# Kernel tuning notes

Hardware: AMD Instinct MI355X
Metric: run time of the kernel (lower is better)

Reference implementation:

```python
import jax, jax.numpy as jnp
import numpy as np

DEPTH = 6
HEADS = 12
DIM_HEAD = 64
ROT_DIM = 32  # rotary applied to first 32 dims of each head


def _ln(x, g, b, eps=1e-5):
    m = x.mean(-1, keepdims=True)
    v = ((x - m) ** 2).mean(-1, keepdims=True)
    return (x - m) * jax.lax.rsqrt(v + eps) * g + b


def _rope(x, inv_freq):
    # x: [b, h, n, DIM_HEAD]; rotate first ROT_DIM dims, interleaved-pair convention
    n = x.shape[2]
    t = jnp.arange(n, dtype=x.dtype)
    freqs = t[:, None] * inv_freq[None, :]          # [n, ROT_DIM//2]
    freqs = jnp.repeat(freqs, 2, axis=-1)           # [n, ROT_DIM]
    cos, sin = jnp.cos(freqs), jnp.sin(freqs)
    x1, x2 = x[..., :ROT_DIM], x[..., ROT_DIM:]
    xr = x1.reshape(*x1.shape[:-1], ROT_DIM // 2, 2)
    half = jnp.stack([-xr[..., 1], xr[..., 0]], axis=-1).reshape(x1.shape)
    return jnp.concatenate([x1 * cos + half * sin, x2], axis=-1)


def setup_inputs() -> dict:
    key = jax.random.key(0)
    ks = jax.random.split(key, 16)
    b, n, pd, d, mlp = 2, 1023, 768, 768, 3072
    inner = HEADS * DIM_HEAD
    s = 0.02
    inp = {}
    inp['filaments'] = jax.random.normal(ks[0], (b, n, pd), jnp.float32)
    inp['mask'] = jnp.ones((b, HEADS, n + 1, n + 1), jnp.float32)
    # patch embedding: LN -> Linear -> LN
    inp['ln_p1_g'] = jnp.ones((pd,), jnp.float32)
    inp['ln_p1_b'] = jnp.zeros((pd,), jnp.float32)
    inp['W_patch'] = jax.random.normal(ks[1], (pd, d), jnp.float32) * s
    inp['b_patch'] = jnp.zeros((d,), jnp.float32)
    inp['ln_p2_g'] = jnp.ones((d,), jnp.float32)
    inp['ln_p2_b'] = jnp.zeros((d,), jnp.float32)
    # PEG depthwise conv1d, k=3
    inp['peg_w'] = jax.random.normal(ks[2], (d, 1, 3), jnp.float32) * s
    inp['peg_b'] = jnp.zeros((d,), jnp.float32)
    inp['cls_token'] = jax.random.normal(ks[3], (1, 1, d), jnp.float32)
    # shared attention (weight-tied across depth)
    inp['ln_a_g'] = jnp.ones((DEPTH, d), jnp.float32)
    inp['ln_a_b'] = jnp.zeros((DEPTH, d), jnp.float32)
    inp['W_qkv'] = jax.random.normal(ks[4], (d, 3 * inner), jnp.float32) * s
    inp['W_o'] = jax.random.normal(ks[5], (inner, d), jnp.float32) * s
    inp['b_o'] = jnp.zeros((d,), jnp.float32)
    inp['inv_freq'] = (1.0 / (10000.0 ** (jnp.arange(0, ROT_DIM, 2, dtype=jnp.float32) / ROT_DIM)))
    # per-layer FFN
    inp['ln_f_g'] = jnp.ones((DEPTH, d), jnp.float32)
    inp['ln_f_b'] = jnp.zeros((DEPTH, d), jnp.float32)
    inp['W1'] = jax.random.normal(ks[6], (DEPTH, d, mlp), jnp.float32) * s
    inp['b1'] = jnp.zeros((DEPTH, mlp), jnp.float32)
    inp['W2'] = jax.random.normal(ks[7], (DEPTH, mlp, d), jnp.float32) * s
    inp['b2'] = jnp.zeros((DEPTH, d), jnp.float32)
    return inp


def reference(filaments, mask, ln_p1_g, ln_p1_b, W_patch, b_patch, ln_p2_g, ln_p2_b,
              peg_w, peg_b, cls_token, ln_a_g, ln_a_b, W_qkv, W_o, b_o, inv_freq,
              ln_f_g, ln_f_b, W1, b1, W2, b2):
    b = filaments.shape[0]
    d = W_patch.shape[1]
    x = _ln(filaments, ln_p1_g, ln_p1_b) @ W_patch + b_patch
    x = _ln(x, ln_p2_g, ln_p2_b)
    x = jnp.concatenate([jnp.broadcast_to(cls_token, (b, 1, d)), x], axis=1)  # [b, n+1, d]
    # PEG: depthwise conv over sequence, residual add
    xc = jnp.transpose(x, (0, 2, 1))  # NCW
    peg = jax.lax.conv_general_dilated(xc, peg_w, (1,), 'SAME',
                                       dimension_numbers=('NCH', 'OIH', 'NCH'),
                                       feature_group_count=d)
    x = x + jnp.transpose(peg, (0, 2, 1)) + peg_b
    add_mask = (1.0 - mask) * (-1e9)
    scale = DIM_HEAD ** -0.5
    n1 = x.shape[1]
    for i in range(DEPTH):
        h = _ln(x, ln_a_g[i], ln_a_b[i])
        qkv = h @ W_qkv
        q, k, v = jnp.split(qkv, 3, axis=-1)
        def to_heads(t):
            return t.reshape(b, n1, HEADS, DIM_HEAD).transpose(0, 2, 1, 3)
        q, k, v = to_heads(q), to_heads(k), to_heads(v)
        q = _rope(q, inv_freq)
        k = _rope(k, inv_freq)
        dots = jnp.einsum('bhid,bhjd->bhij', q, k) * scale + add_mask
        attn = jax.nn.softmax(dots, axis=-1)
        o = jnp.einsum('bhij,bhjd->bhid', attn, v).transpose(0, 2, 1, 3).reshape(b, n1, -1)
        x = o @ W_o + b_o + x
        h = _ln(x, ln_f_g[i], ln_f_b[i])
        x = jax.nn.gelu(h @ W1[i] + b1[i], approximate=False) @ W2[i] + b2[i] + x
    return x
```

## Files before the change

kernel.cpp:

```cpp
#include <hip/hip_runtime.h>
#include <hip/hip_bf16.h>
#include <math.h>

typedef __attribute__((ext_vector_type(8))) short          bf16x8;
typedef __attribute__((ext_vector_type(8))) unsigned short ushort8;
typedef __attribute__((ext_vector_type(4))) float          f32x4;

__device__ __forceinline__ unsigned short f2bf(float f) {
    union { float f; unsigned u; } v; v.f = f;
    unsigned u = v.u;
    unsigned r = (u + 0x7FFFu + ((u >> 16) & 1u)) >> 16;
    return (unsigned short)r;
}
__device__ __forceinline__ float bf2f(unsigned short h) {
    union { unsigned u; float f; } v; v.u = ((unsigned)h) << 16;
    return v.f;
}

__device__ __forceinline__ void gload16(const void* g, void* l) {
    __builtin_amdgcn_global_load_lds(
        (const __attribute__((address_space(1))) void*)g,
        (__attribute__((address_space(3))) void*)l, 16, 0, 0);
}

__global__ __launch_bounds__(256) void wt_cast_k(const float* __restrict__ in,
                                                 unsigned short* __restrict__ out,
                                                 int K, int N) {
    __shared__ float t[64][65];
    in  += (size_t)blockIdx.z * K * N;
    out += (size_t)blockIdx.z * K * N;
    int n0 = blockIdx.x * 64, k0 = blockIdx.y * 64;
    int tx = threadIdx.x & 63, ty = threadIdx.x >> 6;
    #pragma unroll
    for (int p = 0; p < 16; ++p) {
        int k = ty + p * 4;
        t[k][tx] = in[(size_t)(k0 + k) * N + n0 + tx];
    }
    __syncthreads();
    #pragma unroll
    for (int p = 0; p < 16; ++p) {
        int n = ty + p * 4;
        out[(size_t)(n0 + n) * K + k0 + tx] = f2bf(t[tx][n]);
    }
}

__global__ __launch_bounds__(256) void cossin_k(const float* __restrict__ inv_freq,
                                                float* __restrict__ cosT,
                                                float* __restrict__ sinT) {
    int idx = blockIdx.x * 256 + threadIdx.x;
    int t = idx >> 4, p = idx & 15;
    float fr = (float)t * inv_freq[p];
    cosT[idx] = cosf(fr);
    sinT[idx] = sinf(fr);
}

__global__ __launch_bounds__(256) void mask_flags_k(const float* __restrict__ mask,
                                                    unsigned char* __restrict__ flags) {
    int idx = blockIdx.x;
    int tid = threadIdx.x;
    int kt = idx & 15, qt = (idx >> 4) & 15, bh = idx >> 8;
    int r = tid >> 2, cc = (tid & 3) * 16;
    const float* prow = mask + ((size_t)bh * 1024 + (size_t)qt * 64 + r) * 1024 + kt * 64 + cc;
    int bad = 0;
    #pragma unroll
    for (int j = 0; j < 4; ++j) {
        float4 v = *(const float4*)(prow + j * 4);
        bad |= (v.x != 1.f) || (v.y != 1.f) || (v.z != 1.f) || (v.w != 1.f);
    }
    __shared__ int sb[4];
    unsigned long long anyb = __ballot(bad != 0);
    if ((tid & 63) == 0) sb[tid >> 6] = (anyb != 0ull) ? 1 : 0;
    __syncthreads();
    if (tid == 0) flags[idx] = (unsigned char)(!(sb[0] | sb[1] | sb[2] | sb[3]));
}

__global__ __launch_bounds__(256) void ln768_bf_k(const float* __restrict__ in,
                                                  const float* __restrict__ g,
                                                  const float* __restrict__ b,
                                                  unsigned short* __restrict__ out,
                                                  int Mvalid) {
    int r = blockIdx.x, tid = threadIdx.x;
    unsigned short* y = out + (size_t)r * 768;
    if (r >= Mvalid) { y[tid] = 0; y[tid + 256] = 0; y[tid + 512] = 0; return; }
    const float* x = in + (size_t)r * 768;
    float v0 = x[tid], v1 = x[tid + 256], v2 = x[tid + 512];
    __shared__ float red[4];
    float s = v0 + v1 + v2;
    #pragma unroll
    for (int off = 32; off > 0; off >>= 1) s += __shfl_down(s, off);
    if ((tid & 63) == 0) red[tid >> 6] = s;
    __syncthreads();
    float mean = (red[0] + red[1] + red[2] + red[3]) * (1.0f / 768.0f);
    float d0 = v0 - mean, d1 = v1 - mean, d2 = v2 - mean;
    float q = d0 * d0 + d1 * d1 + d2 * d2;
    __syncthreads();
    #pragma unroll
    for (int off = 32; off > 0; off >>= 1) q += __shfl_down(q, off);
    if ((tid & 63) == 0) red[tid >> 6] = q;
    __syncthreads();
    float var = (red[0] + red[1] + red[2] + red[3]) * (1.0f / 768.0f);
    float rs = rsqrtf(var + 1e-5f);
    y[tid]       = f2bf(d0 * rs * g[tid]       + b[tid]);
    y[tid + 256] = f2bf(d1 * rs * g[tid + 256] + b[tid + 256]);
    y[tid + 512] = f2bf(d2 * rs * g[tid + 512] + b[tid + 512]);
}

__global__ __launch_bounds__(256) void ln768_k(const float* __restrict__ in,
                                               const float* __restrict__ g,
                                               const float* __restrict__ b,
                                               float* __restrict__ out,
                                               int remap) {
    int r = blockIdx.x, tid = threadIdx.x;
    const float* x = in + (size_t)r * 768;
    float v0 = x[tid], v1 = x[tid + 256], v2 = x[tid + 512];
    __shared__ float red[4];
    float s = v0 + v1 + v2;
    #pragma unroll
    for (int off = 32; off > 0; off >>= 1) s += __shfl_down(s, off);
    if ((tid & 63) == 0) red[tid >> 6] = s;
    __syncthreads();
    float mean = (red[0] + red[1] + red[2] + red[3]) * (1.0f / 768.0f);
    float d0 = v0 - mean, d1 = v1 - mean, d2 = v2 - mean;
    float q = d0 * d0 + d1 * d1 + d2 * d2;
    __syncthreads();
    #pragma unroll
    for (int off = 32; off > 0; off >>= 1) q += __shfl_down(q, off);
    if ((tid & 63) == 0) red[tid >> 6] = q;
    __syncthreads();
    float var = (red[0] + red[1] + red[2] + red[3]) * (1.0f / 768.0f);
    float rs = rsqrtf(var + 1e-5f);
    int orow = remap ? ((r / 1023) * 1024 + 1 + (r % 1023)) : r;
    float* y = out + (size_t)orow * 768;
    y[tid]       = d0 * rs * g[tid]       + b[tid];
    y[tid + 256] = d1 * rs * g[tid + 256] + b[tid + 256];
    y[tid + 512] = d2 * rs * g[tid + 512] + b[tid + 512];
}

__global__ void cls_k(const float* __restrict__ cls, float* __restrict__ x) {
    int bi = blockIdx.x, tid = threadIdx.x;
    #pragma unroll
    for (int k = 0; k < 3; ++k)
        x[(size_t)bi * 1024 * 768 + tid + k * 256] = cls[tid + k * 256];
}

__global__ __launch_bounds__(256) void peg_ln_k(const float* __restrict__ x,
                                                const float* __restrict__ w,
                                                const float* __restrict__ pb,
                                                float* __restrict__ y,
                                                const float* __restrict__ g,
                                                const float* __restrict__ b,
                                                unsigned short* __restrict__ obf) {
    int r = blockIdx.x;
    int i = r & 1023;
    int tid = threadIdx.x;
    const float* xr = x + (size_t)r * 768;
    float* yr = y + (size_t)r * 768;
    float v[3];
    #pragma unroll
    for (int k = 0; k < 3; ++k) {
        int d = tid + k * 256;
        float c  = xr[d];
        float lf = (i > 0)    ? xr[d - 768] : 0.f;
        float rt = (i < 1023) ? xr[d + 768] : 0.f;
        v[k] = c + pb[d] + w[d * 3 + 0] * lf + w[d * 3 + 1] * c + w[d * 3 + 2] * rt;
        yr[d] = v[k];
    }
    __shared__ float red[4];
    float s = v[0] + v[1] + v[2];
    #pragma unroll
    for (int off = 32; off > 0; off >>= 1) s += __shfl_down(s, off);
    if ((tid & 63) == 0) red[tid >> 6] = s;
    __syncthreads();
    float mean = (red[0] + red[1] + red[2] + red[3]) * (1.0f / 768.0f);
    float d0 = v[0] - mean, d1 = v[1] - mean, d2 = v[2] - mean;
    float q = d0 * d0 + d1 * d1 + d2 * d2;
    __syncthreads();
    #pragma unroll
    for (int off = 32; off > 0; off >>= 1) q += __shfl_down(q, off);
    if ((tid & 63) == 0) red[tid >> 6] = q;
    __syncthreads();
    float var = (red[0] + red[1] + red[2] + red[3]) * (1.0f / 768.0f);
    float rs = rsqrtf(var + 1e-5f);
    unsigned short* yb = obf + (size_t)r * 768;
    yb[tid]       = f2bf(d0 * rs * g[tid]       + b[tid]);
    yb[tid + 256] = f2bf(d1 * rs * g[tid + 256] + b[tid + 256]);
    yb[tid + 512] = f2bf(d2 * rs * g[tid + 512] + b[tid + 512]);
}

__global__ __launch_bounds__(256) void attn_mfma_k(const unsigned short* __restrict__ qkv,
                                                   const float* __restrict__ mask,
                                                   const unsigned char* __restrict__ flags,
                                                   unsigned short* __restrict__ o) {
    const int qt = blockIdx.x, bh = blockIdx.y;
    const int bi = bh / 12, h = bh % 12;
    const int tid = threadIdx.x;
    const int w = tid >> 6, lane = tid & 63;
    const int l16 = lane & 15, lq = lane >> 4;

    __shared__ unsigned short lK[64 * 64];
    __shared__ unsigned short lV[64 * 64];

    const int q0 = qt * 64;
    const size_t tokbase = (size_t)bi * 1024;
    const int qrow = q0 + w * 16 + l16;

    bf16x8 qb[2];
    {
        const unsigned short* qp = qkv + (tokbase + qrow) * 2304 + h * 64;
        qb[0] = *(const bf16x8*)(qp + lq * 8);
        qb[1] = *(const bf16x8*)(qp + 32 + lq * 8);
    }

    const float* mrow = mask + ((size_t)bh * 1024 + qrow) * 1024;
    const unsigned char* fl = flags + ((size_t)bh * 16 + qt) * 16;

    float m_run = -1e30f, l_run = 0.f;
    f32x4 oacc[4] = {};

    for (int kt = 0; kt < 16; ++kt) {
        const int k0 = kt * 64;
        const bool triv = fl[kt] != 0;
        {
            const unsigned short* krp = qkv + (tokbase + k0 + lane) * 2304 + 768 + h * 64 + w * 16;
            const unsigned short* vrp = krp + 768;
            ushort8 kA = *(const ushort8*)krp, kB = *(const ushort8*)(krp + 8);
            ushort8 vA = *(const ushort8*)vrp, vB = *(const ushort8*)(vrp + 8);
            int byA = lane * 128 + ((w * 32 +  0) ^ ((lane & 7) << 4));
            int byB = lane * 128 + ((w * 32 + 16) ^ ((lane & 7) << 4));
            *(ushort8*)((char*)lK + byA) = kA;
            *(ushort8*)((char*)lK + byB) = kB;
            #pragma unroll
            for (int j = 0; j < 16; ++j) {
                int row = w * 16 + j;
                int by = row * 128 + ((2 * lane) ^ ((row & 7) << 4));
                *(unsigned short*)((char*)lV + by) = (j < 8) ? (unsigned short)vA[j] : (unsigned short)vB[j - 8];
            }
        }
        __syncthreads();

        f32x4 sacc[4] = {};
        #pragma unroll
        for (int f = 0; f < 4; ++f) {
            int krow = f * 16 + l16;
            #pragma unroll
            for (int s = 0; s < 2; ++s) {
                int by = krow * 128 + (((s * 64) + lq * 16) ^ ((krow & 7) << 4));
                bf16x8 af = *(const bf16x8*)((const char*)lK + by);
                sacc[f] = __builtin_amdgcn_mfma_f32_16x16x32_bf16(af, qb[s], sacc[f], 0, 0, 0);
            }
        }

        float pv[4][4];
        float smax = -1e30f;
        if (triv) {
            #pragma unroll
            for (int f = 0; f < 4; ++f) {
                pv[f][0] = sacc[f][0] * 0.125f;
                pv[f][1] = sacc[f][1] * 0.125f;
                pv[f][2] = sacc[f][2] * 0.125f;
                pv[f][3] = sacc[f][3] * 0.125f;
                smax = fmaxf(smax, fmaxf(fmaxf(pv[f][0], pv[f][1]), fmaxf(pv[f][2], pv[f][3])));
            }
        } else {
            #pragma unroll
            for (int f = 0; f < 4; ++f) {
                float4 mk = *(const float4*)(mrow + k0 + f * 16 + lq * 4);
                pv[f][0] = sacc[f][0] * 0.125f + (1.f - mk.x) * -1e9f;
                pv[f][1] = sacc[f][1] * 0.125f + (1.f - mk.y) * -1e9f;
                pv[f][2] = sacc[f][2] * 0.125f + (1.f - mk.z) * -1e9f;
                pv[f][3] = sacc[f][3] * 0.125f + (1.f - mk.w) * -1e9f;
                smax = fmaxf(smax, fmaxf(fmaxf(pv[f][0], pv[f][1]), fmaxf(pv[f][2], pv[f][3])));
            }
        }
        smax = fmaxf(smax, __shfl_xor(smax, 16));
        smax = fmaxf(smax, __shfl_xor(smax, 32));
        float m_new = fmaxf(m_run, smax);
        float fac = expf(m_run - m_new);
        float lsum = 0.f;
        #pragma unroll
        for (int f = 0; f < 4; ++f) {
            #pragma unroll
            for (int i = 0; i < 4; ++i) {
                pv[f][i] = expf(pv[f][i] - m_new);
                lsum += pv[f][i];
            }
        }
        lsum += __shfl_xor(lsum, 16);
        lsum += __shfl_xor(lsum, 32);
        l_run = l_run * fac + lsum;
        m_run = m_new;

        #pragma unroll
        for (int i = 0; i < 4; ++i) {
            float fi = __shfl(fac, 4 * lq + i);
            oacc[0][i] *= fi; oacc[1][i] *= fi; oacc[2][i] *= fi; oacc[3][i] *= fi;
        }

        unsigned wpk[4][2];
        #pragma unroll
        for (int f = 0; f < 4; ++f) {
            wpk[f][0] = (unsigned)f2bf(pv[f][0]) | ((unsigned)f2bf(pv[f][1]) << 16);
            wpk[f][1] = (unsigned)f2bf(pv[f][2]) | ((unsigned)f2bf(pv[f][3]) << 16);
        }

        #pragma unroll
        for (int s = 0; s < 2; ++s) {
            unsigned aw[4];
            #pragma unroll
            for (int t = 0; t < 4; ++t) {
                int src = (2 * (lq & 1) + (t >> 1)) * 16 + l16;
                unsigned lo = __shfl(wpk[2 * s][t & 1], src);
                unsigned hi = __shfl(wpk[2 * s + 1][t & 1], src);
                aw[t] = (lq >> 1) ? hi : lo;
            }
            union { unsigned u[4]; bf16x8 v; } pa;
            pa.u[0] = aw[0]; pa.u[1] = aw[1]; pa.u[2] = aw[2]; pa.u[3] = aw[3];
            #pragma unroll
            for (int f = 0; f < 4; ++f) {
                int drow = f * 16 + l16;
                int by = drow * 128 + (((s * 64) + lq * 16) ^ ((drow & 7) << 4));
                bf16x8 vb = *(const bf16x8*)((const char*)lV + by);
                oacc[f] = __builtin_amdgcn_mfma_f32_16x16x32_bf16(pa.v, vb, oacc[f], 0, 0, 0);
            }
        }
        __syncthreads();
    }

    #pragma unroll
    for (int i = 0; i < 4; ++i) {
        float li = __shfl(l_run, 4 * lq + i);
        float inv = 1.f / li;
        int row = q0 + w * 16 + 4 * lq + i;
        unsigned short* op = o + (tokbase + row) * 768 + h * 64 + l16;
        #pragma unroll
        for (int f = 0; f < 4; ++f)
            op[f * 16] = f2bf(oacc[f][i] * inv);
    }
}

template<bool GELU, bool OBF16, bool ROPE>
__global__ __launch_bounds__(256) void gemm64_k(const unsigned short* __restrict__ A,
                                                const unsigned short* __restrict__ Bt,
                                                const float* __restrict__ bias,
                                                const float* __restrict__ res,
                                                void* __restrict__ Cv,
                                                const float* __restrict__ cosT,
                                                const float* __restrict__ sinT,
                                                int M, int N, int K) {
    __shared__ unsigned short lA[2][64 * 64];
    __shared__ unsigned short lB[2][64 * 64];
    int tid = threadIdx.x;
    int m0 = blockIdx.y * 64, n0 = blockIdx.x * 64;
    int w = tid >> 6, lane = tid & 63;
    int l16 = lane & 15, lq = lane >> 4;
    int wrow = (w >> 1) * 32, wcol = (w & 1) * 32;

    f32x4 acc[2][2] = {};

    auto stage = [&](int buf, int k0) {
        #pragma unroll
        for (int i = 0; i < 2; ++i) {
            int ch = tid + i * 256;
            int r = ch >> 3, c = ch & 7;
            int cs = c ^ (r & 7);
            gload16(A + (size_t)(m0 + r) * K + k0 + cs * 8, &lA[buf][ch * 8]);
        }
        #pragma unroll
        for (int i = 0; i < 2; ++i) {
            int ch = tid + i * 256;
            int r = ch >> 3, c = ch & 7;
            int cs = c ^ (r & 7);
            gload16(Bt + (size_t)(n0 + r) * K + k0 + cs * 8, &lB[buf][ch * 8]);
        }
    };

    const int nk = K >> 6;
    stage(0, 0);
    __syncthreads();
    int cur = 0;
    for (int t = 0; t < nk; ++t) {
        if (t + 1 < nk) stage(cur ^ 1, (t + 1) << 6);
        #pragma unroll
        for (int ks = 0; ks < 2; ++ks) {
            bf16x8 af[2], bfv[2];
            #pragma unroll
            for (int fm = 0; fm < 2; ++fm) {
                int row = wrow + fm * 16 + l16;
                int by = row * 128 + ((ks * 64 + lq * 16) ^ ((row & 7) << 4));
                af[fm] = *(const bf16x8*)((const char*)&lA[cur][0] + by);
            }
            #pragma unroll
            for (int fn = 0; fn < 2; ++fn) {
                int row = wcol + fn * 16 + l16;
                int by = row * 128 + ((ks * 64 + lq * 16) ^ ((row & 7) << 4));
                bfv[fn] = *(const bf16x8*)((const char*)&lB[cur][0] + by);
            }
            #pragma unroll
            for (int fm = 0; fm < 2; ++fm)
                #pragma unroll
                for (int fn = 0; fn < 2; ++fn)
                    acc[fm][fn] = __builtin_amdgcn_mfma_f32_16x16x32_bf16(af[fm], bfv[fn], acc[fm][fn], 0, 0, 0);
        }
        __syncthreads();
        cur ^= 1;
    }

    float* Cf = (float*)Cv;
    unsigned short* Cb = (unsigned short*)Cv;
    #pragma unroll
    for (int fm = 0; fm < 2; ++fm)
        #pragma unroll
        for (int fn = 0; fn < 2; ++fn) {
            int col = n0 + wcol + fn * 16 + l16;
            float bv = bias ? bias[col] : 0.f;
            bool rot = ROPE && (col < 1536) && ((wcol + fn * 16) < 32);
            int pidx = (wcol + fn * 16 + l16) >> 1;
            #pragma unroll
            for (int i = 0; i < 4; ++i) {
                int row = m0 + wrow + fm * 16 + 4 * lq + i;
                float v = acc[fm][fn][i];
                if (ROPE) {
                    float pr = __shfl_xor(v, 1);
                    if (rot) {
                        int tt = (row & 1023) * 16 + pidx;
                        float c = cosT[tt], s = sinT[tt];
                        v = (l16 & 1) ? (v * c + pr * s) : (v * c - pr * s);
                    }
                }
                if (row < M) {
                    v += bv;
                    if (GELU) v = 0.5f * v * (1.0f + erff(v * 0.70710678118f));
                    if (res)  v += res[(size_t)row * N + col];
                    if (OBF16) Cb[(size_t)row * N + col] = f2bf(v);
                    else       Cf[(size_t)row * N + col] = v;
                }
            }
        }
}

__global__ __launch_bounds__(256) void gemm64_splitk_k(const unsigned short* __restrict__ A,
                                                       const unsigned short* __restrict__ Bt,
                                                       float* __restrict__ P,
                                                       int M, int N, int Ktot, int Kc) {
    __shared__ unsigned short lA[2][64 * 64];
    __shared__ unsigned short lB[2][64 * 64];
    int tid = threadIdx.x;
    int m0 = blockIdx.y * 64, n0 = blockIdx.x * 64;
    int kb = blockIdx.z * Kc;
    int w = tid >> 6, lane = tid & 63;
    int l16 = lane & 15, lq = lane >> 4;
    int wrow = (w >> 1) * 32, wcol = (w & 1) * 32;

    f32x4 acc[2][2] = {};

    auto stage = [&](int buf, int k0) {
        #pragma unroll
        for (int i = 0; i < 2; ++i) {
            int ch = tid + i * 256;
            int r = ch >> 3, c = ch & 7;
            int cs = c ^ (r & 7);
            gload16(A + (size_t)(m0 + r) * Ktot + k0 + cs * 8, &lA[buf][ch * 8]);
        }
        #pragma unroll
        for (int i = 0; i < 2; ++i) {
            int ch = tid + i * 256;
            int r = ch >> 3, c = ch & 7;
            int cs = c ^ (r & 7);
            gload16(Bt + (size_t)(n0 + r) * Ktot + k0 + cs * 8, &lB[buf][ch * 8]);
        }
    };

    const int nk = Kc >> 6;
    stage(0, kb);
    __syncthreads();
    int cur = 0;
    for (int t = 0; t < nk; ++t) {
        if (t + 1 < nk) stage(cur ^ 1, kb + ((t + 1) << 6));
        #pragma unroll
        for (int ks = 0; ks < 2; ++ks) {
            bf16x8 af[2], bfv[2];
            #pragma unroll
            for (int fm = 0; fm < 2; ++fm) {
                int row = wrow + fm * 16 + l16;
                int by = row * 128 + ((ks * 64 + lq * 16) ^ ((row & 7) << 4));
                af[fm] = *(const bf16x8*)((const char*)&lA[cur][0] + by);
            }
            #pragma unroll
            for (int fn = 0; fn < 2; ++fn) {
                int row = wcol + fn * 16 + l16;
                int by = row * 128 + ((ks * 64 + lq * 16) ^ ((row & 7) << 4));
                bfv[fn] = *(const bf16x8*)((const char*)&lB[cur][0] + by);
            }
            #pragma unroll
            for (int fm = 0; fm < 2; ++fm)
                #pragma unroll
                for (int fn = 0; fn < 2; ++fn)
                    acc[fm][fn] = __builtin_amdgcn_mfma_f32_16x16x32_bf16(af[fm], bfv[fn], acc[fm][fn], 0, 0, 0);
        }
        __syncthreads();
        cur ^= 1;
    }

    float* Pz = P + (size_t)blockIdx.z * M * N;
    #pragma unroll
    for (int fm = 0; fm < 2; ++fm)
        #pragma unroll
        for (int fn = 0; fn < 2; ++fn) {
            int col = n0 + wcol + fn * 16 + l16;
            #pragma unroll
            for (int i = 0; i < 4; ++i) {
                int row = m0 + wrow + fm * 16 + 4 * lq + i;
                Pz[(size_t)row * N + col] = acc[fm][fn][i];
            }
        }
}

template<int NP>
__global__ __launch_bounds__(256) void redsum_ln_k(const float* __restrict__ P,
                                                   const float* __restrict__ bias,
                                                   const float* __restrict__ res,
                                                   float* __restrict__ outf,
                                                   const float* __restrict__ g,
                                                   const float* __restrict__ b,
                                                   unsigned short* __restrict__ obf) {
    const int MN = 2048 * 768;
    int r = blockIdx.x, tid = threadIdx.x;
    float v[3];
    #pragma unroll
    for (int j = 0; j < 3; ++j) {
        int col = tid + j * 256;
        size_t idx = (size_t)r * 768 + col;
        float a = res[idx] + bias[col];
        #pragma unroll
        for (int pz = 0; pz < NP; ++pz)
            a += P[(size_t)pz * MN + idx];
        v[j] = a;
        outf[idx] = a;
    }
    if (!g) return;
    __shared__ float red[4];
    float s = v[0] + v[1] + v[2];
    #pragma unroll
    for (int off = 32; off > 0; off >>= 1) s += __shfl_down(s, off);
    if ((tid & 63) == 0) red[tid >> 6] = s;
    __syncthreads();
    float mean = (red[0] + red[1] + red[2] + red[3]) * (1.0f / 768.0f);
    float d0 = v[0] - mean, d1 = v[1] - mean, d2 = v[2] - mean;
    float q = d0 * d0 + d1 * d1 + d2 * d2;
    __syncthreads();
    #pragma unroll
    for (int off = 32; off > 0; off >>= 1) q += __shfl_down(q, off);
    if ((tid & 63) == 0) red[tid >> 6] = q;
    __syncthreads();
    float var = (red[0] + red[1] + red[2] + red[3]) * (1.0f / 768.0f);
    float rs = rsqrtf(var + 1e-5f);
    unsigned short* yb = obf + (size_t)r * 768;
    yb[tid]       = f2bf(d0 * rs * g[tid]       + b[tid]);
    yb[tid + 256] = f2bf(d1 * rs * g[tid + 256] + b[tid + 256]);
    yb[tid + 512] = f2bf(d2 * rs * g[tid + 512] + b[tid + 512]);
}

extern "C" void kernel_launch(void* const* d_in, const int* in_sizes, int n_in,
                              void* d_out, int out_size, void* d_ws, size_t ws_size,
                              hipStream_t stream) {
    const float* filaments = (const float*)d_in[0];
    const float* mask      = (const float*)d_in[1];
    const float* ln_p1_g   = (const float*)d_in[2];
    const float* ln_p1_b   = (const float*)d_in[3];
    const float* W_patch   = (const float*)d_in[4];
    const float* b_patch   = (const float*)d_in[5];
    const float* ln_p2_g   = (const float*)d_in[6];
    const float* ln_p2_b   = (const float*)d_in[7];
    const float* peg_w     = (const float*)d_in[8];
    const float* peg_b     = (const float*)d_in[9];
    const float* cls_token = (const float*)d_in[10];
    const float* ln_a_g    = (const float*)d_in[11];
    const float* ln_a_b    = (const float*)d_in[12];
    const float* W_qkv     = (const float*)d_in[13];
    const float* W_o       = (const float*)d_in[14];
    const float* b_o       = (const float*)d_in[15];
    const float* inv_freq  = (const float*)d_in[16];
    const float* ln_f_g    = (const float*)d_in[17];
    const float* ln_f_b    = (const float*)d_in[18];
    const float* W1        = (const float*)d_in[19];
    const float* b1        = (const float*)d_in[20];
    const float* W2        = (const float*)d_in[21];
    const float* b2        = (const float*)d_in[22];

    char* p = (char*)d_ws;
    float* xa            = (float*)p;          p += 2048 * 768 * 4;
    float* xb            = (float*)p;          p += 2048 * 768 * 4;
    unsigned short* h_bf = (unsigned short*)p; p += 2048 * 768 * 2;
    unsigned short* qkv  = (unsigned short*)p; p += 2048 * 3072 * 2;
    float* Pbuf          = (float*)p;          p += (size_t)4 * 2048 * 768 * 4;
    unsigned short* w1t  = (unsigned short*)p; p += (size_t)6 * 3072 * 768 * 2;
    unsigned short* w2t  = (unsigned short*)p; p += (size_t)6 * 3072 * 768 * 2;
    unsigned short* wqt  = (unsigned short*)p; p += 2304 * 768 * 2;
    unsigned short* wot  = (unsigned short*)p; p += 768 * 768 * 2;
    unsigned short* wpt  = (unsigned short*)p; p += 768 * 768 * 2;
    float* cosT          = (float*)p;          p += 16384 * 4;
    float* sinT          = (float*)p;          p += 16384 * 4;
    unsigned char* flags = (unsigned char*)p;  p += 8192;
    unsigned short* m_bf = qkv;
    float* tmp = (float*)qkv;
    float* out = (float*)d_out;

    mask_flags_k<<<6144, 256, 0, stream>>>(mask, flags);
    cossin_k<<<64, 256, 0, stream>>>(inv_freq, cosT, sinT);
    wt_cast_k<<<dim3(12, 12), 256, 0, stream>>>(W_patch, wpt, 768, 768);
    wt_cast_k<<<dim3(36, 12), 256, 0, stream>>>(W_qkv,  wqt, 768, 2304);
    wt_cast_k<<<dim3(12, 12), 256, 0, stream>>>(W_o,    wot, 768, 768);
    wt_cast_k<<<dim3(48, 12, 6), 256, 0, stream>>>(W1, w1t, 768, 3072);
    wt_cast_k<<<dim3(12, 48, 6), 256, 0, stream>>>(W2, w2t, 3072, 768);

    ln768_bf_k<<<2048, 256, 0, stream>>>(filaments, ln_p1_g, ln_p1_b, h_bf, 2046);
    gemm64_k<false, false, false><<<dim3(12, 32), 256, 0, stream>>>(h_bf, wpt, b_patch, nullptr, tmp,
                                                                    nullptr, nullptr, 2046, 768, 768);
    ln768_k<<<2046, 256, 0, stream>>>(tmp, ln_p2_g, ln_p2_b, xa, 1);
    cls_k<<<2, 256, 0, stream>>>(cls_token, xa);
    peg_ln_k<<<2048, 256, 0, stream>>>(xa, peg_w, peg_b, xb, ln_a_g, ln_a_b, h_bf);

    float* cur = xb;
    float* nxt = xa;
    for (int i = 0; i < 6; ++i) {
        gemm64_k<false, true, true><<<dim3(36, 32), 256, 0, stream>>>(h_bf, wqt, nullptr, nullptr, qkv,
                                                                      cosT, sinT, 2048, 2304, 768);
        attn_mfma_k<<<dim3(16, 24), 256, 0, stream>>>(qkv, mask, flags, h_bf);
        gemm64_splitk_k<<<dim3(12, 32, 2), 256, 0, stream>>>(h_bf, wot, Pbuf, 2048, 768, 768, 384);
        redsum_ln_k<2><<<2048, 256, 0, stream>>>(Pbuf, b_o, cur, nxt,
                                                 ln_f_g + i * 768, ln_f_b + i * 768, h_bf);
        gemm64_k<true, true, false><<<dim3(48, 32), 256, 0, stream>>>(h_bf, w1t + (size_t)i * 3072 * 768, b1 + i * 3072,
                                                                      nullptr, m_bf, nullptr, nullptr, 2048, 3072, 768);
        gemm64_splitk_k<<<dim3(12, 32, 4), 256, 0, stream>>>(m_bf, w2t + (size_t)i * 768 * 3072, Pbuf, 2048, 768, 3072, 768);
        redsum_ln_k<4><<<2048, 256, 0, stream>>>(Pbuf, b2 + i * 768, nxt, (i == 5) ? out : cur,
                                                 (i < 5) ? (ln_a_g + (i + 1) * 768) : nullptr,
                                                 (i < 5) ? (ln_a_b + (i + 1) * 768) : nullptr, h_bf);
    }
}
```

Baseline: 941.6 us.

## Use three-stage LDS pipeline with explicit vmcnt waits in GEMM kernels

Replaces the double-buffered GEMM main loop with a triple-buffered pipeline that keeps two tiles in flight. It waits with explicit s_waitcnt vmcnt counts plus a single barrier per iteration, where before it synchronised after each compute step. The aim is to hide global-to-LDS load latency behind MFMA work. It raises LDS use to 48KB per block, which may lower occupancy, and it relies on the compiler's vmcnt accounting matching the hand-written counts.

```diff
diff --git a/kernel.cpp b/kernel.cpp
--- a/kernel.cpp
+++ b/kernel.cpp
@@ -338,6 +338,69 @@
     }
 }
 
+#define GEMM64_PIPE(A_, Bt_, KSTRIDE_, KBASE_, NK_)                                   \
+    auto stage = [&](int buf, int t) {                                                \
+        int k0 = (KBASE_) + (t << 6);                                                 \
+        {                                                                             \
+            int ch = tid, r = ch >> 3, c = ch & 7;                                    \
+            int cs = c ^ (r & 7);                                                     \
+            gload16((A_) + (size_t)(m0 + r) * (KSTRIDE_) + k0 + cs * 8,               \
+                    &lA[buf][ch * 8]);                                                \
+        }                                                                             \
+        {                                                                             \
+            int ch = tid + 256, r = ch >> 3, c = ch & 7;                              \
+            int cs = c ^ (r & 7);                                                     \
+            gload16((A_) + (size_t)(m0 + r) * (KSTRIDE_) + k0 + cs * 8,               \
+                    &lA[buf][ch * 8]);                                                \
+        }                                                                             \
+        {                                                                             \
+            int ch = tid, r = ch >> 3, c = ch & 7;                                    \
+            int cs = c ^ (r & 7);                                                     \
+            gload16((Bt_) + (size_t)(n0 + r) * (KSTRIDE_) + k0 + cs * 8,              \
+                    &lB[buf][ch * 8]);                                                \
+        }                                                                             \
+        {                                                                             \
+            int ch = tid + 256, r = ch >> 3, c = ch & 7;                              \
+            int cs = c ^ (r & 7);                                                     \
+            gload16((Bt_) + (size_t)(n0 + r) * (KSTRIDE_) + k0 + cs * 8,              \
+                    &lB[buf][ch * 8]);                                                \
+        }                                                                             \
+    };                                                                                \
+    const int nk = (NK_);                                                             \
+    stage(0, 0);                                                                      \
+    stage(1, 1);                                                                      \
+    int rd = 0, wr = 2;                                                               \
+    for (int t = 0; t < nk; ++t) {                                                    \
+        if (t + 1 < nk) asm volatile("s_waitcnt vmcnt(4)" ::: "memory");              \
+        else            asm volatile("s_waitcnt vmcnt(0)" ::: "memory");              \
+        __builtin_amdgcn_s_barrier();                                                 \
+        if (t + 2 < nk) stage(wr, t + 2);                                             \
+        _Pragma("unroll")                                                             \
+        for (int ks = 0; ks < 2; ++ks) {                                              \
+            bf16x8 af[2], bfv[2];                                                     \
+            _Pragma("unroll")                                                         \
+            for (int fm = 0; fm < 2; ++fm) {                                          \
+                int row = wrow + fm * 16 + l16;                                       \
+                int by = row * 128 + ((ks * 64 + lq * 16) ^ ((row & 7) << 4));        \
+                af[fm] = *(const bf16x8*)((const char*)&lA[rd][0] + by);              \
+            }                                                                         \
+            _Pragma("unroll")                                                         \
+            for (int fn = 0; fn < 2; ++fn) {                                          \
+                int row = wcol + fn * 16 + l16;                                       \
+                int by = row * 128 + ((ks * 64 + lq * 16) ^ ((row & 7) << 4));        \
+                bfv[fn] = *(const bf16x8*)((const char*)&lB[rd][0] + by);             \
+            }                                                                         \
+            _Pragma("unroll")                                                         \
+            for (int fm = 0; fm < 2; ++fm)                                            \
+                _Pragma("unroll")                                                     \
+                for (int fn = 0; fn < 2; ++fn)                                        \
+                    acc[fm][fn] = __builtin_amdgcn_mfma_f32_16x16x32_bf16(            \
+                        af[fm], bfv[fn], acc[fm][fn], 0, 0, 0);                       \
+        }                                                                             \
+        rd = (rd == 2) ? 0 : rd + 1;                                                  \
+        wr = (wr == 2) ? 0 : wr + 1;                                                  \
+    }
+
 template<bool GELU, bool OBF16, bool ROPE>
 __global__ __launch_bounds__(256) void gemm64_k(const unsigned short* __restrict__ A,
                                                 const unsigned short* __restrict__ Bt,
@@ -347,8 +410,8 @@
                                                 const float* __restrict__ cosT,
                                                 const float* __restrict__ sinT,
                                                 int M, int N, int K) {
-    __shared__ unsigned short lA[2][64 * 64];
-    __shared__ unsigned short lB[2][64 * 64];
+    __shared__ unsigned short lA[3][64 * 64];
+    __shared__ unsigned short lB[3][64 * 64];
     int tid = threadIdx.x;
     int m0 = blockIdx.y * 64, n0 = blockIdx.x * 64;
     int w = tid >> 6, lane = tid & 63;
@@ -357,53 +420,7 @@
 
     f32x4 acc[2][2] = {};
 
-    auto stage = [&](int buf, int k0) {
-        #pragma unroll
-        for (int i = 0; i < 2; ++i) {
-            int ch = tid + i * 256;
-            int r = ch >> 3, c = ch & 7;
-            int cs = c ^ (r & 7);
-            gload16(A + (size_t)(m0 + r) * K + k0 + cs * 8, &lA[buf][ch * 8]);
-        }
-        #pragma unroll
-        for (int i = 0; i < 2; ++i) {
-            int ch = tid + i * 256;
-            int r = ch >> 3, c = ch & 7;
-            int cs = c ^ (r & 7);
-            gload16(Bt + (size_t)(n0 + r) * K + k0 + cs * 8, &lB[buf][ch * 8]);
-        }
-    };
-
-    const int nk = K >> 6;
-    stage(0, 0);
-    __syncthreads();
-    int cur = 0;
-    for (int t = 0; t < nk; ++t) {
-        if (t + 1 < nk) stage(cur ^ 1, (t + 1) << 6);
-        #pragma unroll
-        for (int ks = 0; ks < 2; ++ks) {
-            bf16x8 af[2], bfv[2];
-            #pragma unroll
-            for (int fm = 0; fm < 2; ++fm) {
-                int row = wrow + fm * 16 + l16;
-                int by = row * 128 + ((ks * 64 + lq * 16) ^ ((row & 7) << 4));
-                af[fm] = *(const bf16x8*)((const char*)&lA[cur][0] + by);
-            }
-            #pragma unroll
-            for (int fn = 0; fn < 2; ++fn) {
-                int row = wcol + fn * 16 + l16;
-                int by = row * 128 + ((ks * 64 + lq * 16) ^ ((row & 7) << 4));
-                bfv[fn] = *(const bf16x8*)((const char*)&lB[cur][0] + by);
-            }
-            #pragma unroll
-            for (int fm = 0; fm < 2; ++fm)
-                #pragma unroll
-                for (int fn = 0; fn < 2; ++fn)
-                    acc[fm][fn] = __builtin_amdgcn_mfma_f32_16x16x32_bf16(af[fm], bfv[fn], acc[fm][fn], 0, 0, 0);
-        }
-        __syncthreads();
-        cur ^= 1;
-    }
+    GEMM64_PIPE(A, Bt, K, 0, K >> 6)
 
     float* Cf = (float*)Cv;
     unsigned short* Cb = (unsigned short*)Cv;
@@ -442,8 +459,8 @@
                                                        const unsigned short* __restrict__ Bt,
                                                        float* __restrict__ P,
                                                        int M, int N, int Ktot, int Kc) {
-    __shared__ unsigned short lA[2][64 * 64];
-    __shared__ unsigned short lB[2][64 * 64];
+    __shared__ unsigned short lA[3][64 * 64];
+    __shared__ unsigned short lB[3][64 * 64];
     int tid = threadIdx.x;
     int m0 = blockIdx.y * 64, n0 = blockIdx.x * 64;
     int kb = blockIdx.z * Kc;
@@ -453,53 +470,7 @@
 
     f32x4 acc[2][2] = {};
 
-    auto stage = [&](int buf, int k0) {
-        #pragma unroll
-        for (int i = 0; i < 2; ++i) {
-            int ch = tid + i * 256;
-            int r = ch >> 3, c = ch & 7;
-            int cs = c ^ (r & 7);
-            gload16(A + (size_t)(m0 + r) * Ktot + k0 + cs * 8, &lA[buf][ch * 8]);
-        }
-        #pragma unroll
-        for (int i = 0; i < 2; ++i) {
-            int ch = tid + i * 256;
-            int r = ch >> 3, c = ch & 7;
-            int cs = c ^ (r & 7);
-            gload16(Bt + (size_t)(n0 + r) * Ktot + k0 + cs * 8, &lB[buf][ch * 8]);
-        }
-    };
-
-    const int nk = Kc >> 6;
-    stage(0, kb);
-    __syncthreads();
-    int cur = 0;
-    for (int t = 0; t < nk; ++t) {
-        if (t + 1 < nk) stage(cur ^ 1, kb + ((t + 1) << 6));
-        #pragma unroll
-        for (int ks = 0; ks < 2; ++ks) {
-            bf16x8 af[2], bfv[2];
-            #pragma unroll
-            for (int fm = 0; fm < 2; ++fm) {
-                int row = wrow + fm * 16 + l16;
-                int by = row * 128 + ((ks * 64 + lq * 16) ^ ((row & 7) << 4));
-                af[fm] = *(const bf16x8*)((const char*)&lA[cur][0] + by);
-            }
-            #pragma unroll
-            for (int fn = 0; fn < 2; ++fn) {
-                int row = wcol + fn * 16 + l16;
-                int by = row * 128 + ((ks * 64 + lq * 16) ^ ((row & 7) << 4));
-                bfv[fn] = *(const bf16x8*)((const char*)&lB[cur][0] + by);
-            }
-            #pragma unroll
-            for (int fm = 0; fm < 2; ++fm)
-                #pragma unroll
-                for (int fn = 0; fn < 2; ++fn)
-                    acc[fm][fn] = __builtin_amdgcn_mfma_f32_16x16x32_bf16(af[fm], bfv[fn], acc[fm][fn], 0, 0, 0);
-        }
-        __syncthreads();
-        cur ^= 1;
-    }
+    GEMM64_PIPE(A, Bt, Ktot, kb, Kc >> 6)
 
     float* Pz = P + (size_t)blockIdx.z * M * N;
     #pragma unroll
```

After: 966.2 us. 2.6% more time.

## Double-buffer K/V tiles in attention kernel to overlap global loads with MFMA

Applied to the files above, without the earlier changes.

The attention kernel now keeps two LDS buffers each for K and V. The next tile's global loads are issued into registers before the QK^T and PV MFMAs on the current tile, and are written to the alternate buffer afterwards. This hides global load latency behind compute and removes one __syncthreads per iteration. In exchange it doubles LDS use to 32KB per block, which may lower occupancy, and keeps the prefetched values live in registers across the compute.

```diff
diff --git a/kernel.cpp b/kernel.cpp
--- a/kernel.cpp
+++ b/kernel.cpp
@@ -197,8 +197,8 @@
     const int w = tid >> 6, lane = tid & 63;
     const int l16 = lane & 15, lq = lane >> 4;
 
-    __shared__ unsigned short lK[64 * 64];
-    __shared__ unsigned short lV[64 * 64];
+    __shared__ unsigned short lK[2][64 * 64];
+    __shared__ unsigned short lV[2][64 * 64];
 
     const int q0 = qt * 64;
     const size_t tokbase = (size_t)bi * 1024;
@@ -214,29 +214,38 @@
     const float* mrow = mask + ((size_t)bh * 1024 + qrow) * 1024;
     const unsigned char* fl = flags + ((size_t)bh * 16 + qt) * 16;
 
+    const int byA = lane * 128 + ((w * 32 +  0) ^ ((lane & 7) << 4));
+    const int byB = lane * 128 + ((w * 32 + 16) ^ ((lane & 7) << 4));
+
     float m_run = -1e30f, l_run = 0.f;
     f32x4 oacc[4] = {};
 
+    {
+        const unsigned short* krp = qkv + (tokbase + lane) * 2304 + 768 + h * 64 + w * 16;
+        ushort8 kA = *(const ushort8*)krp, kB = *(const ushort8*)(krp + 8);
+        ushort8 vA = *(const ushort8*)(krp + 768), vB = *(const ushort8*)(krp + 776);
+        *(ushort8*)((char*)&lK[0][0] + byA) = kA;
+        *(ushort8*)((char*)&lK[0][0] + byB) = kB;
+        #pragma unroll
+        for (int j = 0; j < 16; ++j) {
+            int row = w * 16 + j;
+            int by = row * 128 + ((2 * lane) ^ ((row & 7) << 4));
+            *(unsigned short*)((char*)&lV[0][0] + by) = (j < 8) ? (unsigned short)vA[j] : (unsigned short)vB[j - 8];
+        }
+    }
+
     for (int kt = 0; kt < 16; ++kt) {
-        const int k0 = kt * 64;
+        const int cur = kt & 1;
         const bool triv = fl[kt] != 0;
-        {
-            const unsigned short* krp = qkv + (tokbase + k0 + lane) * 2304 + 768 + h * 64 + w * 16;
-            const unsigned short* vrp = krp + 768;
-            ushort8 kA = *(const ushort8*)krp, kB = *(const ushort8*)(krp + 8);
-            ushort8 vA = *(const ushort8*)vrp, vB = *(const ushort8*)(vrp + 8);
-            int byA = lane * 128 + ((w * 32 +  0) ^ ((lane & 7) << 4));
-            int byB = lane * 128 + ((w * 32 + 16) ^ ((lane & 7) << 4));
-            *(ushort8*)((char*)lK + byA) = kA;
-            *(ushort8*)((char*)lK + byB) = kB;
-            #pragma unroll
-            for (int j = 0; j < 16; ++j) {
-                int row = w * 16 + j;
-                int by = row * 128 + ((2 * lane) ^ ((row & 7) << 4));
-                *(unsigned short*)((char*)lV + by) = (j < 8) ? (unsigned short)vA[j] : (unsigned short)vB[j - 8];
-            }
-        }
         __syncthreads();
+
+        ushort8 kA, kB, vA, vB;
+        const bool have_next = (kt + 1) < 16;
+        if (have_next) {
+            const unsigned short* krp = qkv + (tokbase + (kt + 1) * 64 + lane) * 2304 + 768 + h * 64 + w * 16;
+            kA = *(const ushort8*)krp;       kB = *(const ushort8*)(krp + 8);
+            vA = *(const ushort8*)(krp + 768); vB = *(const ushort8*)(krp + 776);
+        }
 
         f32x4 sacc[4] = {};
         #pragma unroll
@@ -245,7 +254,7 @@
             #pragma unroll
             for (int s = 0; s < 2; ++s) {
                 int by = krow * 128 + (((s * 64) + lq * 16) ^ ((krow & 7) << 4));
-                bf16x8 af = *(const bf16x8*)((const char*)lK + by);
+                bf16x8 af = *(const bf16x8*)((const char*)&lK[cur][0] + by);
                 sacc[f] = __builtin_amdgcn_mfma_f32_16x16x32_bf16(af, qb[s], sacc[f], 0, 0, 0);
             }
         }
@@ -264,7 +273,7 @@
         } else {
             #pragma unroll
             for (int f = 0; f < 4; ++f) {
-                float4 mk = *(const float4*)(mrow + k0 + f * 16 + lq * 4);
+                float4 mk = *(const float4*)(mrow + kt * 64 + f * 16 + lq * 4);
                 pv[f][0] = sacc[f][0] * 0.125f + (1.f - mk.x) * -1e9f;
                 pv[f][1] = sacc[f][1] * 0.125f + (1.f - mk.y) * -1e9f;
                 pv[f][2] = sacc[f][2] * 0.125f + (1.f - mk.z) * -1e9f;
@@ -319,11 +328,22 @@
             for (int f = 0; f < 4; ++f) {
                 int drow = f * 16 + l16;
                 int by = drow * 128 + (((s * 64) + lq * 16) ^ ((drow & 7) << 4));
-                bf16x8 vb = *(const bf16x8*)((const char*)lV + by);
+                bf16x8 vb = *(const bf16x8*)((const char*)&lV[cur][0] + by);
                 oacc[f] = __builtin_amdgcn_mfma_f32_16x16x32_bf16(pa.v, vb, oacc[f], 0, 0, 0);
             }
         }
-        __syncthreads();
+
+        if (have_next) {
+            const int nxt = cur ^ 1;
+            *(ushort8*)((char*)&lK[nxt][0] + byA) = kA;
+            *(ushort8*)((char*)&lK[nxt][0] + byB) = kB;
+            #pragma unroll
+            for (int j = 0; j < 16; ++j) {
+                int row = w * 16 + j;
+                int by = row * 128 + ((2 * lane) ^ ((row & 7) << 4));
+                *(unsigned short*)((char*)&lV[nxt][0] + by) = (j < 8) ? (unsigned short)vA[j] : (unsigned short)vB[j - 8];
+            }
+        }
     }
 
     #pragma unroll
```

Result: faster. 914.6 us (-2.9%).
